# Optimization experiments

Hardware: AMD Instinct MI355X
Metric: run time of the kernel (lower is better)

Reference implementation:

```python
import jax, jax.numpy as jnp
import numpy as np

EPS = 1e-9  # Dice BatchNormalization epsilon


def dice(x, alpha):
    # Keras BatchNormalization(axis=-1, center=False, scale=False) in training
    # mode: normalize over all axes except the last using batch statistics.
    mean = jnp.mean(x, axis=(0, 1), keepdims=True)
    var = jnp.var(x, axis=(0, 1), keepdims=True)
    x_normed = (x - mean) * jax.lax.rsqrt(var + EPS)
    p = jax.nn.sigmoid(x_normed)
    return alpha * (1.0 - p) * x + p * x


def setup_inputs() -> dict:
    key = jax.random.key(0)
    ks = jax.random.split(key, 11)
    B, T, D = 512, 2048, 20
    keys_ = jax.random.normal(ks[0], (B, T, D), dtype=jnp.float32)
    query = jax.random.normal(ks[1], (B, 1, D), dtype=jnp.float32)
    mask = jax.random.randint(ks[2], (B, T), 0, 2) > 0
    # DNN tower weights: hidden dims 80 -> 32 -> 16, attention head 16 -> 1
    W0 = jax.random.normal(ks[3], (80, 32), dtype=jnp.float32) * 0.1
    b0 = jax.random.normal(ks[4], (32,), dtype=jnp.float32) * 0.1
    a0 = jax.random.normal(ks[5], (32,), dtype=jnp.float32) * 0.1
    W1 = jax.random.normal(ks[6], (32, 16), dtype=jnp.float32) * 0.1
    b1 = jax.random.normal(ks[7], (16,), dtype=jnp.float32) * 0.1
    a1 = jax.random.normal(ks[8], (16,), dtype=jnp.float32) * 0.1
    wk = jax.random.normal(ks[9], (16, 1), dtype=jnp.float32) * 0.1
    bk = jax.random.normal(ks[10], (1,), dtype=jnp.float32) * 0.1
    return {"keys": keys_, "query": query, "mask": mask,
            "W0": W0, "b0": b0, "a0": a0,
            "W1": W1, "b1": b1, "a1": a1,
            "wk": wk, "bk": bk}


def reference(keys, query, mask, W0, b0, a0, W1, b1, a1, wk, bk):
    B, T, D = keys.shape
    # repeat query along the key/time axis: [B,1,D] -> [B,T,D]
    queries = jnp.broadcast_to(query, (B, T, D))
    # local-activation features: [B,T,4D] = [B,T,80]
    att = jnp.concatenate([queries, keys, queries - keys, queries * keys], axis=-1)
    # DNN tower with Dice activations (dropout is identity at inference)
    h = dice(att @ W0 + b0, a0)   # [B,T,32]
    h = dice(h @ W1 + b1, a1)     # [B,T,16]
    score = h @ wk + bk           # [B,T,1]
    outputs = jnp.transpose(score, (0, 2, 1))  # [B,1,T]
    # NOTE: the original code computes the masked scores into self.outputs but
    # then (weight_normalization=False, return_score=False) overwrites it with
    # matmul(outputs, keys) using the UNMASKED scores -- we reproduce that.
    return jnp.matmul(outputs, keys)  # [B,1,D]
```

## Files before the change

kernel.cpp:

```cpp
#include <hip/hip_runtime.h>


#define BB 512
#define TT 2048
#define DD 20
#define C0 32
#define C1 16

#define NTH 256
#define NPOS 4
#define POSB (NTH * NPOS)
#define NBLK (TT / POSB)

#define WS_SUM0 0
#define WS_SQ0 32
#define WS_SUM1 64
#define WS_SQ1 80
#define WS_SCALE0 96
#define WS_SHIFT0 128
#define WS_SCALE1 160
#define WS_SHIFT1 176
#define WS_BLOB 192
#define BLOB_J 24
#define BLOB_B (C0 * BLOB_J)

#define PIN(x) asm volatile("" : "+v"(x))

__device__ __forceinline__ float fast_sigmoid(float x) {
    return __builtin_amdgcn_rcpf(1.0f + __expf(-x));
}

__device__ __forceinline__ void load_krow(const float* __restrict__ row,
                                          float* kk) {
    const float4* kr = (const float4*)row;
    float4 a = kr[0], b = kr[1], c = kr[2], d = kr[3], e = kr[4];
    kk[0] = a.x; kk[1] = a.y; kk[2] = a.z; kk[3] = a.w;
    kk[4] = b.x; kk[5] = b.y; kk[6] = b.z; kk[7] = b.w;
    kk[8] = c.x; kk[9] = c.y; kk[10] = c.z; kk[11] = c.w;
    kk[12] = d.x; kk[13] = d.y; kk[14] = d.z; kk[15] = d.w;
    kk[16] = e.x; kk[17] = e.y; kk[18] = e.z; kk[19] = e.w;
}

__global__ void prep_kernel(const float* __restrict__ query,
                            const float* __restrict__ W0,
                            const float* __restrict__ b0,
                            float* __restrict__ blob) {
    const int b = blockIdx.x * 2 + (threadIdx.x >> 5);
    const int j = threadIdx.x & 31;
    float cj = b0[j];
    float* dst = blob + (size_t)b * BLOB_B + j * BLOB_J;
#pragma unroll
    for (int d = 0; d < DD; ++d) {
        float w_q = W0[d * C0 + j];
        float w_k = W0[(DD + d) * C0 + j];
        float w_d = W0[(2 * DD + d) * C0 + j];
        float w_p = W0[(3 * DD + d) * C0 + j];
        float qd = query[b * DD + d];
        dst[d] = w_k - w_d + qd * w_p;
        cj = fmaf(qd, w_q + w_d, cj);
    }
    dst[20] = cj;
}

__global__ __launch_bounds__(256, 2) void pass1_kernel(
    const float* __restrict__ keys, const float* __restrict__ blob,
    float* __restrict__ ws) {
    const int b = blockIdx.x >> 2, chunk = blockIdx.x & 3;
    const int tid = threadIdx.x, wave = tid >> 6, lane = tid & 63;
    const int j0 = wave * 8;
    const float* wb = blob + (size_t)b * BLOB_B;
    const float* kbase = keys + ((size_t)b * TT + chunk * (TT / 4)) * DD;

    float wM[8][DD], cj8[8];
#pragma unroll
    for (int jj = 0; jj < 8; ++jj) {
        load_krow(wb + (j0 + jj) * BLOB_J, wM[jj]);
        cj8[jj] = wb[(j0 + jj) * BLOB_J + 20];
    }
#pragma unroll
    for (int jj = 0; jj < 8; ++jj) {
        PIN(cj8[jj]);
#pragma unroll
        for (int d = 0; d < DD; ++d) PIN(wM[jj][d]);
    }

    float s[8], q[8];
#pragma unroll
    for (int v = 0; v < 8; ++v) { s[v] = 0.f; q[v] = 0.f; }

#pragma unroll 1
    for (int it = 0; it < (TT / 4) / 64; ++it) {
        float kk[DD];
        load_krow(kbase + (size_t)(it * 64 + lane) * DD, kk);
#pragma unroll
        for (int jj = 0; jj < 8; ++jj) {
            float h = cj8[jj];
#pragma unroll
            for (int d = 0; d < DD; ++d) h = fmaf(kk[d], wM[jj][d], h);
            s[jj] += h;
            q[jj] = fmaf(h, h, q[jj]);
        }
    }
    float mine = 0.f;
#pragma unroll
    for (int v = 0; v < 16; ++v) {
        float val = (v < 8) ? s[v] : q[v - 8];
#pragma unroll
        for (int o = 32; o >= 1; o >>= 1) val += __shfl_xor(val, o);
        if (lane == v) mine = val;
    }
    __shared__ float red[64];
    if (lane < 16) {
        int j = j0 + (lane & 7);
        red[(lane < 8 ? 0 : 32) + j] = mine;
    }
    __syncthreads();
    if (tid < 64) atomicAdd(&ws[WS_SUM0 + tid], red[tid]);
}

__global__ void finalize_kernel(float* __restrict__ ws, int nch, int sumOff,
                                int sqOff, int scOff, int shOff) {
    int j = threadIdx.x;
    if (j < nch) {
        const float invN = 1.0f / (float)(BB * TT);
        float mean = ws[sumOff + j] * invN;
        float ex2 = ws[sqOff + j] * invN;
        float var = ex2 - mean * mean;
        float sc = rsqrtf(var + 1e-9f);
        ws[scOff + j] = sc;
        ws[shOff + j] = -mean * sc;
    }
}

#define STAGE_WEIGHTS()                                                      \
    for (int idx = tid; idx < C0 * 24; idx += NTH) {                         \
        int j = idx / 24, r = idx - j * 24;                                  \
        float v;                                                             \
        if (r < 21) v = blob[(size_t)b * BLOB_B + j * BLOB_J + r];           \
        else if (r == 21) v = ws[WS_SCALE0 + j];                             \
        else if (r == 22) v = ws[WS_SHIFT0 + j];                             \
        else v = a0[j];                                                      \
        lw[idx] = v;                                                         \
    }                                                                        \
    for (int idx = tid; idx < C0 * C1; idx += NTH) lw1[idx] = W1[idx];

#define LOAD_AND_PIN_KEYS()                                                  \
    const float* kbase = keys + ((size_t)b * TT + chunk * POSB) * DD;        \
    float kk[NPOS][DD];                                                      \
    _Pragma("unroll") for (int pp = 0; pp < NPOS; ++pp)                      \
        load_krow(kbase + (size_t)(tid + pp * NTH) * DD, kk[pp]);            \
    _Pragma("unroll") for (int pp = 0; pp < NPOS; ++pp)                      \
        _Pragma("unroll") for (int d = 0; d < DD; ++d) PIN(kk[pp][d]);

#define TOWER_JLOOP()                                                        \
    _Pragma("unroll 1") for (int j = 0; j < C0; ++j) {                       \
        const float4* wv = (const float4*)&lw[j * 24];                       \
        float4 A = wv[0], B = wv[1], Cc = wv[2], E = wv[3], F = wv[4],       \
               P = wv[5];                                                    \
        const float4* uv = (const float4*)&lw1[j * C1];                      \
        float4 U0 = uv[0], U1 = uv[1], U2 = uv[2], U3 = uv[3];               \
        float wr[DD] = {A.x,  A.y,  A.z,  A.w,  B.x,  B.y,  B.z,             \
                        B.w,  Cc.x, Cc.y, Cc.z, Cc.w, E.x,  E.y,             \
                        E.z,  E.w,  F.x,  F.y,  F.z,  F.w};                  \
        float ur[C1] = {U0.x, U0.y, U0.z, U0.w, U1.x, U1.y, U1.z, U1.w,      \
                        U2.x, U2.y, U2.z, U2.w, U3.x, U3.y, U3.z, U3.w};     \
        float h[NPOS];                                                       \
        _Pragma("unroll") for (int pp = 0; pp < NPOS; ++pp) {                \
            float hh = P.x;                                                  \
            _Pragma("unroll") for (int d = 0; d < DD; ++d)                   \
                hh = fmaf(kk[pp][d], wr[d], hh);                             \
            h[pp] = hh;                                                      \
        }                                                                    \
        _Pragma("unroll") for (int pp = 0; pp < NPOS; ++pp) {                \
            float pr = fast_sigmoid(fmaf(h[pp], P.y, P.z));                  \
            float h0d = h[pp] * (P.w + pr * (1.0f - P.w));                   \
            _Pragma("unroll") for (int c = 0; c < C1; ++c)                   \
                h1[pp][c] = fmaf(h0d, ur[c], h1[pp][c]);                     \
        }                                                                    \
    }

__global__ __launch_bounds__(NTH, 2) void pass2_kernel(
    const float* __restrict__ keys, const float* __restrict__ blob,
    const float* __restrict__ a0, const float* __restrict__ W1,
    const float* __restrict__ b1, float* __restrict__ ws) {
    const int b = blockIdx.x >> 1, chunk = blockIdx.x & 1;
    const int tid = threadIdx.x, wave = tid >> 6, lane = tid & 63;
    __shared__ float lw[C0 * 24];
    __shared__ float lw1[C0 * C1];
    __shared__ float red[4][32];
    STAGE_WEIGHTS()
    __syncthreads();

    LOAD_AND_PIN_KEYS()

    float h1[NPOS][C1];
#pragma unroll
    for (int pp = 0; pp < NPOS; ++pp)
#pragma unroll
        for (int c = 0; c < C1; ++c) h1[pp][c] = 0.f;

    TOWER_JLOOP()

    float s1[C1], q1[C1];
#pragma unroll
    for (int c = 0; c < C1; ++c) {
        float bc = b1[c], sv = 0.f, qv = 0.f;
#pragma unroll
        for (int pp = 0; pp < NPOS; ++pp) {
            float v = h1[pp][c] + bc;
            sv += v;
            qv = fmaf(v, v, qv);
        }
        s1[c] = sv;
        q1[c] = qv;
    }
    float mine = 0.f;
#pragma unroll
    for (int v = 0; v < 32; ++v) {
        float val = (v < C1) ? s1[v] : q1[v - C1];
#pragma unroll
        for (int o = 32; o >= 1; o >>= 1) val += __shfl_xor(val, o);
        if (lane == v) mine = val;
    }
    if (lane < 32) red[wave][lane] = mine;
    __syncthreads();
    if (tid < 32)
        atomicAdd(&ws[WS_SUM1 + tid],
                  red[0][tid] + red[1][tid] + red[2][tid] + red[3][tid]);
}

__global__ __launch_bounds__(NTH, 2) void pass3_kernel(
    const float* __restrict__ keys, const float* __restrict__ blob,
    const float* __restrict__ a0, const float* __restrict__ W1,
    const float* __restrict__ b1, const float* __restrict__ a1,
    const float* __restrict__ wk, const float* __restrict__ bk,
    const float* __restrict__ ws, float* __restrict__ out) {
    const int b = blockIdx.x >> 1, chunk = blockIdx.x & 1;
    const int tid = threadIdx.x, wave = tid >> 6, lane = tid & 63;
    __shared__ float lw[C0 * 24];
    __shared__ float lw1[C0 * C1];
    __shared__ float ld1[C1 * 4];
    __shared__ float red[4][DD];
    STAGE_WEIGHTS()
    if (tid < C1) {
        ld1[tid * 4 + 0] = ws[WS_SCALE1 + tid];
        ld1[tid * 4 + 1] = ws[WS_SHIFT1 + tid];
        ld1[tid * 4 + 2] = a1[tid];
        ld1[tid * 4 + 3] = wk[tid];
    }
    __syncthreads();

    LOAD_AND_PIN_KEYS()

    float h1[NPOS][C1];
#pragma unroll
    for (int pp = 0; pp < NPOS; ++pp)
#pragma unroll
        for (int c = 0; c < C1; ++c) h1[pp][c] = 0.f;

    TOWER_JLOOP()

    const float bkv = bk[0];
    float oacc[DD];
#pragma unroll
    for (int d = 0; d < DD; ++d) oacc[d] = 0.f;
#pragma unroll
    for (int pp = 0; pp < NPOS; ++pp) {
        float score = bkv;
#pragma unroll
        for (int c = 0; c < C1; ++c) {
            float v = h1[pp][c] + b1[c];
            float pr = fast_sigmoid(fmaf(v, ld1[c * 4 + 0], ld1[c * 4 + 1]));
            float al = ld1[c * 4 + 2];
            float hd = v * (al + pr * (1.0f - al));
            score = fmaf(hd, ld1[c * 4 + 3], score);
        }
#pragma unroll
        for (int d = 0; d < DD; ++d) oacc[d] = fmaf(score, kk[pp][d], oacc[d]);
    }
    float mine = 0.f;
#pragma unroll
    for (int v = 0; v < DD; ++v) {
        float val = oacc[v];
#pragma unroll
        for (int o = 32; o >= 1; o >>= 1) val += __shfl_xor(val, o);
        if (lane == v) mine = val;
    }
    if (lane < DD) red[wave][lane] = mine;
    __syncthreads();
    if (tid < DD)
        atomicAdd(&out[b * DD + tid],
                  red[0][tid] + red[1][tid] + red[2][tid] + red[3][tid]);
}

extern "C" void kernel_launch(void* const* d_in, const int* in_sizes, int n_in,
                              void* d_out, int out_size, void* d_ws,
                              size_t ws_size, hipStream_t stream) {
    const float* keys = (const float*)d_in[0];
    const float* query = (const float*)d_in[1];
    const float* W0 = (const float*)d_in[3];
    const float* b0 = (const float*)d_in[4];
    const float* a0 = (const float*)d_in[5];
    const float* W1 = (const float*)d_in[6];
    const float* b1 = (const float*)d_in[7];
    const float* a1 = (const float*)d_in[8];
    const float* wk = (const float*)d_in[9];
    const float* bk = (const float*)d_in[10];
    float* out = (float*)d_out;
    float* ws = (float*)d_ws;
    float* blob = ws + WS_BLOB;

    hipMemsetAsync(ws, 0, 96 * sizeof(float), stream);
    hipMemsetAsync(out, 0, (size_t)out_size * sizeof(float), stream);

    prep_kernel<<<BB / 2, 64, 0, stream>>>(query, W0, b0, blob);

    pass1_kernel<<<BB * 4, 256, 0, stream>>>(keys, blob, ws);
    finalize_kernel<<<1, 32, 0, stream>>>(ws, 32, WS_SUM0, WS_SQ0, WS_SCALE0,
                                          WS_SHIFT0);
    pass2_kernel<<<BB * NBLK, NTH, 0, stream>>>(keys, blob, a0, W1, b1, ws);
    finalize_kernel<<<1, 16, 0, stream>>>(ws, 16, WS_SUM1, WS_SQ1, WS_SCALE1,
                                          WS_SHIFT1);
    pass3_kernel<<<BB * NBLK, NTH, 0, stream>>>(keys, blob, a0, W1, b1, a1, wk,
                                                bk, ws, out);
}
```

Measured before the change: 288.8 us.

## Fuse prep and finalize kernels into passes, stream weights from LDS with prefetch

Removes the separate prep kernel and the two finalize launches: each pass block now folds the query into W0 itself in shared memory and computes the BatchNorm scale and shift from the raw sums. Pass1 no longer pins 160 weight registers; it reads weights from LDS with a one-row software prefetch and double-buffers the key row loads. The tower j-loop likewise prefetches the next weight row from LDS. This cuts launch count and register pressure, at the cost of redundant per-block weight folding and extra LDS traffic.

```diff
diff --git a/kernel.cpp b/kernel.cpp
--- a/kernel.cpp
+++ b/kernel.cpp
@@ -10,19 +10,12 @@
 #define NTH 256
 #define NPOS 4
 #define POSB (NTH * NPOS)
-#define NBLK (TT / POSB)
 
 #define WS_SUM0 0
 #define WS_SQ0 32
 #define WS_SUM1 64
 #define WS_SQ1 80
-#define WS_SCALE0 96
-#define WS_SHIFT0 128
-#define WS_SCALE1 160
-#define WS_SHIFT1 176
-#define WS_BLOB 192
-#define BLOB_J 24
-#define BLOB_B (C0 * BLOB_J)
+#define EPS 1e-9f
 
 #define PIN(x) asm volatile("" : "+v"(x))
 
@@ -41,48 +34,44 @@
     kk[16] = e.x; kk[17] = e.y; kk[18] = e.z; kk[19] = e.w;
 }
 
-__global__ void prep_kernel(const float* __restrict__ query,
-                            const float* __restrict__ W0,
-                            const float* __restrict__ b0,
-                            float* __restrict__ blob) {
-    const int b = blockIdx.x * 2 + (threadIdx.x >> 5);
-    const int j = threadIdx.x & 31;
-    float cj = b0[j];
-    float* dst = blob + (size_t)b * BLOB_B + j * BLOB_J;
-#pragma unroll
-    for (int d = 0; d < DD; ++d) {
-        float w_q = W0[d * C0 + j];
+__device__ __forceinline__ void stage_fold(int b, int tid,
+                                           const float* __restrict__ query,
+                                           const float* __restrict__ W0,
+                                           const float* __restrict__ b0,
+                                           float* lw) {
+    for (int idx = tid; idx < C0 * DD; idx += NTH) {
+        int j = idx & 31, d = idx >> 5;
+        float qd = query[b * DD + d];
         float w_k = W0[(DD + d) * C0 + j];
         float w_d = W0[(2 * DD + d) * C0 + j];
         float w_p = W0[(3 * DD + d) * C0 + j];
-        float qd = query[b * DD + d];
-        dst[d] = w_k - w_d + qd * w_p;
-        cj = fmaf(qd, w_q + w_d, cj);
-    }
-    dst[20] = cj;
-}
-
-__global__ __launch_bounds__(256, 2) void pass1_kernel(
-    const float* __restrict__ keys, const float* __restrict__ blob,
+        lw[j * 24 + d] = w_k - w_d + qd * w_p;
+    }
+    if (tid < C0) {
+        float cj = b0[tid];
+        for (int d = 0; d < DD; ++d) {
+            float qd = query[b * DD + d];
+            cj = fmaf(qd, W0[d * C0 + tid] + W0[(2 * DD + d) * C0 + tid], cj);
+        }
+        lw[tid * 24 + 20] = cj;
+    }
+}
+
+__global__ __launch_bounds__(NTH, 2) void pass1_kernel(
+    const float* __restrict__ keys, const float* __restrict__ query,
+    const float* __restrict__ W0, const float* __restrict__ b0,
     float* __restrict__ ws) {
     const int b = blockIdx.x >> 2, chunk = blockIdx.x & 3;
     const int tid = threadIdx.x, wave = tid >> 6, lane = tid & 63;
     const int j0 = wave * 8;
-    const float* wb = blob + (size_t)b * BLOB_B;
+    __shared__ float lw[C0 * 24];
+    __shared__ float red[64];
+    stage_fold(b, tid, query, W0, b0, lw);
+    __syncthreads();
+
     const float* kbase = keys + ((size_t)b * TT + chunk * (TT / 4)) * DD;
-
-    float wM[8][DD], cj8[8];
-#pragma unroll
-    for (int jj = 0; jj < 8; ++jj) {
-        load_krow(wb + (j0 + jj) * BLOB_J, wM[jj]);
-        cj8[jj] = wb[(j0 + jj) * BLOB_J + 20];
-    }
-#pragma unroll
-    for (int jj = 0; jj < 8; ++jj) {
-        PIN(cj8[jj]);
-#pragma unroll
-        for (int d = 0; d < DD; ++d) PIN(wM[jj][d]);
-    }
+    float kk[DD], kn[DD];
+    load_krow(kbase + (size_t)lane * DD, kk);
 
     float s[8], q[8];
 #pragma unroll
@@ -90,16 +79,36 @@
 
 #pragma unroll 1
     for (int it = 0; it < (TT / 4) / 64; ++it) {
-        float kk[DD];
-        load_krow(kbase + (size_t)(it * 64 + lane) * DD, kk);
+        if (it < (TT / 4) / 64 - 1)
+            load_krow(kbase + (size_t)((it + 1) * 64 + lane) * DD, kn);
+#pragma unroll
+        for (int d = 0; d < DD; ++d) PIN(kk[d]);
+
+        const float4* wv = (const float4*)&lw[j0 * 24];
+        float4 A = wv[0], B = wv[1], C2 = wv[2], D2 = wv[3], E2 = wv[4],
+               F2 = wv[5];
 #pragma unroll
         for (int jj = 0; jj < 8; ++jj) {
-            float h = cj8[jj];
-#pragma unroll
-            for (int d = 0; d < DD; ++d) h = fmaf(kk[d], wM[jj][d], h);
+            float4 nA, nB, nC, nD, nE, nF;
+            if (jj < 7) {
+                const float4* nv = (const float4*)&lw[(j0 + jj + 1) * 24];
+                nA = nv[0]; nB = nv[1]; nC = nv[2];
+                nD = nv[3]; nE = nv[4]; nF = nv[5];
+            }
+            float wr[DD] = {A.x,  A.y,  A.z,  A.w,  B.x,  B.y,  B.z,
+                            B.w,  C2.x, C2.y, C2.z, C2.w, D2.x, D2.y,
+                            D2.z, D2.w, E2.x, E2.y, E2.z, E2.w};
+            float h = F2.x;
+#pragma unroll
+            for (int d = 0; d < DD; ++d) h = fmaf(kk[d], wr[d], h);
             s[jj] += h;
             q[jj] = fmaf(h, h, q[jj]);
+            if (jj < 7) {
+                A = nA; B = nB; C2 = nC; D2 = nD; E2 = nE; F2 = nF;
+            }
         }
+#pragma unroll
+        for (int d = 0; d < DD; ++d) kk[d] = kn[d];
     }
     float mine = 0.f;
 #pragma unroll
@@ -109,7 +118,6 @@
         for (int o = 32; o >= 1; o >>= 1) val += __shfl_xor(val, o);
         if (lane == v) mine = val;
     }
-    __shared__ float red[64];
     if (lane < 16) {
         int j = j0 + (lane & 7);
         red[(lane < 8 ? 0 : 32) + j] = mine;
@@ -118,31 +126,59 @@
     if (tid < 64) atomicAdd(&ws[WS_SUM0 + tid], red[tid]);
 }
 
-__global__ void finalize_kernel(float* __restrict__ ws, int nch, int sumOff,
-                                int sqOff, int scOff, int shOff) {
-    int j = threadIdx.x;
-    if (j < nch) {
+__device__ __forceinline__ void stage_dice0(int tid,
+                                            const float* __restrict__ ws,
+                                            const float* __restrict__ a0,
+                                            float* lw) {
+    if (tid < C0) {
         const float invN = 1.0f / (float)(BB * TT);
-        float mean = ws[sumOff + j] * invN;
-        float ex2 = ws[sqOff + j] * invN;
-        float var = ex2 - mean * mean;
-        float sc = rsqrtf(var + 1e-9f);
-        ws[scOff + j] = sc;
-        ws[shOff + j] = -mean * sc;
-    }
-}
-
-#define STAGE_WEIGHTS()                                                      \
-    for (int idx = tid; idx < C0 * 24; idx += NTH) {                         \
-        int j = idx / 24, r = idx - j * 24;                                  \
-        float v;                                                             \
-        if (r < 21) v = blob[(size_t)b * BLOB_B + j * BLOB_J + r];           \
-        else if (r == 21) v = ws[WS_SCALE0 + j];                             \
-        else if (r == 22) v = ws[WS_SHIFT0 + j];                             \
-        else v = a0[j];                                                      \
-        lw[idx] = v;                                                         \
+        float mean = ws[WS_SUM0 + tid] * invN;
+        float ex2 = ws[WS_SQ0 + tid] * invN;
+        float sc = rsqrtf(ex2 - mean * mean + EPS);
+        lw[tid * 24 + 21] = sc;
+        lw[tid * 24 + 22] = -mean * sc;
+        lw[tid * 24 + 23] = a0[tid];
+    }
+}
+
+#define TOWER_JLOOP()                                                        \
+    float4 cA, cB, cC, cD, cE, cF;                                           \
+    {                                                                        \
+        const float4* wv = (const float4*)&lw[0];                            \
+        cA = wv[0]; cB = wv[1]; cC = wv[2];                                  \
+        cD = wv[3]; cE = wv[4]; cF = wv[5];                                  \
     }                                                                        \
-    for (int idx = tid; idx < C0 * C1; idx += NTH) lw1[idx] = W1[idx];
+    _Pragma("unroll 1") for (int j = 0; j < C0; ++j) {                       \
+        const float4* uv = (const float4*)&lw1[j * C1];                      \
+        float4 U0 = uv[0], U1 = uv[1], U2 = uv[2], U3 = uv[3];               \
+        float4 nA, nB, nC, nD, nE, nF;                                       \
+        if (j < C0 - 1) {                                                    \
+            const float4* nv = (const float4*)&lw[(j + 1) * 24];             \
+            nA = nv[0]; nB = nv[1]; nC = nv[2];                              \
+            nD = nv[3]; nE = nv[4]; nF = nv[5];                              \
+        }                                                                    \
+        float wr[DD] = {cA.x, cA.y, cA.z, cA.w, cB.x, cB.y, cB.z,            \
+                        cB.w, cC.x, cC.y, cC.z, cC.w, cD.x, cD.y,            \
+                        cD.z, cD.w, cE.x, cE.y, cE.z, cE.w};                 \
+        float h[NPOS];                                                       \
+        _Pragma("unroll") for (int pp = 0; pp < NPOS; ++pp) {                \
+            float hh = cF.x;                                                 \
+            _Pragma("unroll") for (int d = 0; d < DD; ++d)                   \
+                hh = fmaf(kk[pp][d], wr[d], hh);                             \
+            h[pp] = hh;                                                      \
+        }                                                                    \
+        float ur[C1] = {U0.x, U0.y, U0.z, U0.w, U1.x, U1.y, U1.z, U1.w,      \
+                        U2.x, U2.y, U2.z, U2.w, U3.x, U3.y, U3.z, U3.w};     \
+        _Pragma("unroll") for (int pp = 0; pp < NPOS; ++pp) {                \
+            float pr = fast_sigmoid(fmaf(h[pp], cF.y, cF.z));                \
+            float h0d = h[pp] * (cF.w + pr * (1.0f - cF.w));                 \
+            _Pragma("unroll") for (int c = 0; c < C1; ++c)                   \
+                h1[pp][c] = fmaf(h0d, ur[c], h1[pp][c]);                     \
+        }                                                                    \
+        if (j < C0 - 1) {                                                    \
+            cA = nA; cB = nB; cC = nC; cD = nD; cE = nE; cF = nF;            \
+        }                                                                    \
+    }
 
 #define LOAD_AND_PIN_KEYS()                                                  \
     const float* kbase = keys + ((size_t)b * TT + chunk * POSB) * DD;        \
@@ -152,35 +188,9 @@
     _Pragma("unroll") for (int pp = 0; pp < NPOS; ++pp)                      \
         _Pragma("unroll") for (int d = 0; d < DD; ++d) PIN(kk[pp][d]);
 
-#define TOWER_JLOOP()                                                        \
-    _Pragma("unroll 1") for (int j = 0; j < C0; ++j) {                       \
-        const float4* wv = (const float4*)&lw[j * 24];                       \
-        float4 A = wv[0], B = wv[1], Cc = wv[2], E = wv[3], F = wv[4],       \
-               P = wv[5];                                                    \
-        const float4* uv = (const float4*)&lw1[j * C1];                      \
-        float4 U0 = uv[0], U1 = uv[1], U2 = uv[2], U3 = uv[3];               \
-        float wr[DD] = {A.x,  A.y,  A.z,  A.w,  B.x,  B.y,  B.z,             \
-                        B.w,  Cc.x, Cc.y, Cc.z, Cc.w, E.x,  E.y,             \
-                        E.z,  E.w,  F.x,  F.y,  F.z,  F.w};                  \
-        float ur[C1] = {U0.x, U0.y, U0.z, U0.w, U1.x, U1.y, U1.z, U1.w,      \
-                        U2.x, U2.y, U2.z, U2.w, U3.x, U3.y, U3.z, U3.w};     \
-        float h[NPOS];                                                       \
-        _Pragma("unroll") for (int pp = 0; pp < NPOS; ++pp) {                \
-            float hh = P.x;                                                  \
-            _Pragma("unroll") for (int d = 0; d < DD; ++d)                   \
-                hh = fmaf(kk[pp][d], wr[d], hh);                             \
-            h[pp] = hh;                                                      \
-        }                                                                    \
-        _Pragma("unroll") for (int pp = 0; pp < NPOS; ++pp) {                \
-            float pr = fast_sigmoid(fmaf(h[pp], P.y, P.z));                  \
-            float h0d = h[pp] * (P.w + pr * (1.0f - P.w));                   \
-            _Pragma("unroll") for (int c = 0; c < C1; ++c)                   \
-                h1[pp][c] = fmaf(h0d, ur[c], h1[pp][c]);                     \
-        }                                                                    \
-    }
-
 __global__ __launch_bounds__(NTH, 2) void pass2_kernel(
-    const float* __restrict__ keys, const float* __restrict__ blob,
+    const float* __restrict__ keys, const float* __restrict__ query,
+    const float* __restrict__ W0, const float* __restrict__ b0,
     const float* __restrict__ a0, const float* __restrict__ W1,
     const float* __restrict__ b1, float* __restrict__ ws) {
     const int b = blockIdx.x >> 1, chunk = blockIdx.x & 1;
@@ -188,7 +198,9 @@
     __shared__ float lw[C0 * 24];
     __shared__ float lw1[C0 * C1];
     __shared__ float red[4][32];
-    STAGE_WEIGHTS()
+    stage_fold(b, tid, query, W0, b0, lw);
+    stage_dice0(tid, ws, a0, lw);
+    for (int idx = tid; idx < C0 * C1; idx += NTH) lw1[idx] = W1[idx];
     __syncthreads();
 
     LOAD_AND_PIN_KEYS()
@@ -230,7 +242,8 @@
 }
 
 __global__ __launch_bounds__(NTH, 2) void pass3_kernel(
-    const float* __restrict__ keys, const float* __restrict__ blob,
+    const float* __restrict__ keys, const float* __restrict__ query,
+    const float* __restrict__ W0, const float* __restrict__ b0,
     const float* __restrict__ a0, const float* __restrict__ W1,
     const float* __restrict__ b1, const float* __restrict__ a1,
     const float* __restrict__ wk, const float* __restrict__ bk,
@@ -241,10 +254,16 @@
     __shared__ float lw1[C0 * C1];
     __shared__ float ld1[C1 * 4];
     __shared__ float red[4][DD];
-    STAGE_WEIGHTS()
+    stage_fold(b, tid, query, W0, b0, lw);
+    stage_dice0(tid, ws, a0, lw);
+    for (int idx = tid; idx < C0 * C1; idx += NTH) lw1[idx] = W1[idx];
     if (tid < C1) {
-        ld1[tid * 4 + 0] = ws[WS_SCALE1 + tid];
-        ld1[tid * 4 + 1] = ws[WS_SHIFT1 + tid];
+        const float invN = 1.0f / (float)(BB * TT);
+        float mean = ws[WS_SUM1 + tid] * invN;
+        float ex2 = ws[WS_SQ1 + tid] * invN;
+        float sc = rsqrtf(ex2 - mean * mean + EPS);
+        ld1[tid * 4 + 0] = sc;
+        ld1[tid * 4 + 1] = -mean * sc;
         ld1[tid * 4 + 2] = a1[tid];
         ld1[tid * 4 + 3] = wk[tid];
     }
@@ -308,19 +327,13 @@
     const float* bk = (const float*)d_in[10];
     float* out = (float*)d_out;
     float* ws = (float*)d_ws;
-    float* blob = ws + WS_BLOB;
 
     hipMemsetAsync(ws, 0, 96 * sizeof(float), stream);
     hipMemsetAsync(out, 0, (size_t)out_size * sizeof(float), stream);
 
-    prep_kernel<<<BB / 2, 64, 0, stream>>>(query, W0, b0, blob);
-
-    pass1_kernel<<<BB * 4, 256, 0, stream>>>(keys, blob, ws);
-    finalize_kernel<<<1, 32, 0, stream>>>(ws, 32, WS_SUM0, WS_SQ0, WS_SCALE0,
-                                          WS_SHIFT0);
-    pass2_kernel<<<BB * NBLK, NTH, 0, stream>>>(keys, blob, a0, W1, b1, ws);
-    finalize_kernel<<<1, 16, 0, stream>>>(ws, 16, WS_SUM1, WS_SQ1, WS_SCALE1,
-                                          WS_SHIFT1);
-    pass3_kernel<<<BB * NBLK, NTH, 0, stream>>>(keys, blob, a0, W1, b1, a1, wk,
-                                                bk, ws, out);
-}
+    pass1_kernel<<<BB * 4, NTH, 0, stream>>>(keys, query, W0, b0, ws);
+    pass2_kernel<<<BB * 2, NTH, 0, stream>>>(keys, query, W0, b0, a0, W1, b1,
+                                             ws);
+    pass3_kernel<<<BB * 2, NTH, 0, stream>>>(keys, query, W0, b0, a0, W1, b1,
+                                             a1, wk, bk, ws, out);
+}
```

New measurement: 313.2 us. +8.5%, slower.

## Fold BN finalize into consumers, read weights directly, restructure pass1 per-thread

Applied to the files above, without the earlier changes.

Drops the two single-block finalize kernels; each consumer block now computes the Dice batch-norm scale and shift from the raw sums itself. The pass2/pass3 tower loop reads layer weights straight from global memory (uniform loads) instead of staging them in LDS. pass1 switches from a wave-per-8-channels layout with a loop over positions to each thread holding two key rows and computing all 32 channels with 64 wave reductions. This removes launch gaps and LDS staging, but adds redundant normalization math per block, more scalar or global weight traffic, and a heavier shuffle reduction in pass1.

```diff
diff --git a/kernel.cpp b/kernel.cpp
--- a/kernel.cpp
+++ b/kernel.cpp
@@ -10,19 +10,15 @@
 #define NTH 256
 #define NPOS 4
 #define POSB (NTH * NPOS)
-#define NBLK (TT / POSB)
 
 #define WS_SUM0 0
 #define WS_SQ0 32
 #define WS_SUM1 64
 #define WS_SQ1 80
-#define WS_SCALE0 96
-#define WS_SHIFT0 128
-#define WS_SCALE1 160
-#define WS_SHIFT1 176
 #define WS_BLOB 192
 #define BLOB_J 24
 #define BLOB_B (C0 * BLOB_J)
+#define EPS 1e-9f
 
 #define PIN(x) asm volatile("" : "+v"(x))
 
@@ -62,87 +58,54 @@
     dst[20] = cj;
 }
 
-__global__ __launch_bounds__(256, 2) void pass1_kernel(
+__global__ __launch_bounds__(NTH, 2) void pass1_kernel(
     const float* __restrict__ keys, const float* __restrict__ blob,
     float* __restrict__ ws) {
     const int b = blockIdx.x >> 2, chunk = blockIdx.x & 3;
     const int tid = threadIdx.x, wave = tid >> 6, lane = tid & 63;
-    const int j0 = wave * 8;
+    const float* kbase = keys + ((size_t)b * TT + chunk * (TT / 4)) * DD;
     const float* wb = blob + (size_t)b * BLOB_B;
-    const float* kbase = keys + ((size_t)b * TT + chunk * (TT / 4)) * DD;
-
-    float wM[8][DD], cj8[8];
-#pragma unroll
-    for (int jj = 0; jj < 8; ++jj) {
-        load_krow(wb + (j0 + jj) * BLOB_J, wM[jj]);
-        cj8[jj] = wb[(j0 + jj) * BLOB_J + 20];
-    }
-#pragma unroll
-    for (int jj = 0; jj < 8; ++jj) {
-        PIN(cj8[jj]);
-#pragma unroll
-        for (int d = 0; d < DD; ++d) PIN(wM[jj][d]);
-    }
-
-    float s[8], q[8];
-#pragma unroll
-    for (int v = 0; v < 8; ++v) { s[v] = 0.f; q[v] = 0.f; }
-
-#pragma unroll 1
-    for (int it = 0; it < (TT / 4) / 64; ++it) {
-        float kk[DD];
-        load_krow(kbase + (size_t)(it * 64 + lane) * DD, kk);
-#pragma unroll
-        for (int jj = 0; jj < 8; ++jj) {
-            float h = cj8[jj];
-#pragma unroll
-            for (int d = 0; d < DD; ++d) h = fmaf(kk[d], wM[jj][d], h);
-            s[jj] += h;
-            q[jj] = fmaf(h, h, q[jj]);
+
+    float kk[2][DD];
+    load_krow(kbase + (size_t)tid * DD, kk[0]);
+    load_krow(kbase + (size_t)(tid + NTH) * DD, kk[1]);
+#pragma unroll
+    for (int pp = 0; pp < 2; ++pp)
+#pragma unroll
+        for (int d = 0; d < DD; ++d) PIN(kk[pp][d]);
+
+    float s[C0], q[C0];
+#pragma unroll
+    for (int j = 0; j < C0; ++j) { s[j] = 0.f; q[j] = 0.f; }
+
+#pragma unroll
+    for (int j = 0; j < C0; ++j) {
+        const float* w = wb + j * BLOB_J;
+        float h0 = w[20], h1v = w[20];
+#pragma unroll
+        for (int d = 0; d < DD; ++d) {
+            h0 = fmaf(kk[0][d], w[d], h0);
+            h1v = fmaf(kk[1][d], w[d], h1v);
         }
+        s[j] += h0 + h1v;
+        q[j] = fmaf(h0, h0, q[j]);
+        q[j] = fmaf(h1v, h1v, q[j]);
     }
     float mine = 0.f;
 #pragma unroll
-    for (int v = 0; v < 16; ++v) {
-        float val = (v < 8) ? s[v] : q[v - 8];
+    for (int v = 0; v < 64; ++v) {
+        float val = (v < C0) ? s[v] : q[v - C0];
 #pragma unroll
         for (int o = 32; o >= 1; o >>= 1) val += __shfl_xor(val, o);
         if (lane == v) mine = val;
     }
-    __shared__ float red[64];
-    if (lane < 16) {
-        int j = j0 + (lane & 7);
-        red[(lane < 8 ? 0 : 32) + j] = mine;
-    }
-    __syncthreads();
-    if (tid < 64) atomicAdd(&ws[WS_SUM0 + tid], red[tid]);
-}
-
-__global__ void finalize_kernel(float* __restrict__ ws, int nch, int sumOff,
-                                int sqOff, int scOff, int shOff) {
-    int j = threadIdx.x;
-    if (j < nch) {
-        const float invN = 1.0f / (float)(BB * TT);
-        float mean = ws[sumOff + j] * invN;
-        float ex2 = ws[sqOff + j] * invN;
-        float var = ex2 - mean * mean;
-        float sc = rsqrtf(var + 1e-9f);
-        ws[scOff + j] = sc;
-        ws[shOff + j] = -mean * sc;
-    }
-}
-
-#define STAGE_WEIGHTS()                                                      \
-    for (int idx = tid; idx < C0 * 24; idx += NTH) {                         \
-        int j = idx / 24, r = idx - j * 24;                                  \
-        float v;                                                             \
-        if (r < 21) v = blob[(size_t)b * BLOB_B + j * BLOB_J + r];           \
-        else if (r == 21) v = ws[WS_SCALE0 + j];                             \
-        else if (r == 22) v = ws[WS_SHIFT0 + j];                             \
-        else v = a0[j];                                                      \
-        lw[idx] = v;                                                         \
-    }                                                                        \
-    for (int idx = tid; idx < C0 * C1; idx += NTH) lw1[idx] = W1[idx];
+    __shared__ float red[4][64];
+    red[wave][lane] = mine;
+    __syncthreads();
+    if (tid < 64)
+        atomicAdd(&ws[tid],
+                  red[0][tid] + red[1][tid] + red[2][tid] + red[3][tid]);
+}
 
 #define LOAD_AND_PIN_KEYS()                                                  \
     const float* kbase = keys + ((size_t)b * TT + chunk * POSB) * DD;        \
@@ -153,30 +116,33 @@
         _Pragma("unroll") for (int d = 0; d < DD; ++d) PIN(kk[pp][d]);
 
 #define TOWER_JLOOP()                                                        \
-    _Pragma("unroll 1") for (int j = 0; j < C0; ++j) {                       \
-        const float4* wv = (const float4*)&lw[j * 24];                       \
-        float4 A = wv[0], B = wv[1], Cc = wv[2], E = wv[3], F = wv[4],       \
-               P = wv[5];                                                    \
-        const float4* uv = (const float4*)&lw1[j * C1];                      \
-        float4 U0 = uv[0], U1 = uv[1], U2 = uv[2], U3 = uv[3];               \
-        float wr[DD] = {A.x,  A.y,  A.z,  A.w,  B.x,  B.y,  B.z,             \
-                        B.w,  Cc.x, Cc.y, Cc.z, Cc.w, E.x,  E.y,             \
-                        E.z,  E.w,  F.x,  F.y,  F.z,  F.w};                  \
-        float ur[C1] = {U0.x, U0.y, U0.z, U0.w, U1.x, U1.y, U1.z, U1.w,      \
-                        U2.x, U2.y, U2.z, U2.w, U3.x, U3.y, U3.z, U3.w};     \
+    _Pragma("unroll 2") for (int j = 0; j < C0; ++j) {                       \
+        float4 P = ld0[j];            \
+        const float* w = wb + j * BLOB_J;             \
+        const float* u = W1 + j * C1;                 \
         float h[NPOS];                                                       \
         _Pragma("unroll") for (int pp = 0; pp < NPOS; ++pp) {                \
             float hh = P.x;                                                  \
             _Pragma("unroll") for (int d = 0; d < DD; ++d)                   \
-                hh = fmaf(kk[pp][d], wr[d], hh);                             \
+                hh = fmaf(kk[pp][d], w[d], hh);                              \
             h[pp] = hh;                                                      \
         }                                                                    \
         _Pragma("unroll") for (int pp = 0; pp < NPOS; ++pp) {                \
             float pr = fast_sigmoid(fmaf(h[pp], P.y, P.z));                  \
             float h0d = h[pp] * (P.w + pr * (1.0f - P.w));                   \
             _Pragma("unroll") for (int c = 0; c < C1; ++c)                   \
-                h1[pp][c] = fmaf(h0d, ur[c], h1[pp][c]);                     \
+                h1[pp][c] = fmaf(h0d, u[c], h1[pp][c]);                      \
         }                                                                    \
+    }
+
+#define STAGE_DICE0()                                                        \
+    if (tid < C0) {                                                          \
+        const float invN = 1.0f / (float)(BB * TT);                          \
+        float mean = ws[WS_SUM0 + tid] * invN;                               \
+        float ex2 = ws[WS_SQ0 + tid] * invN;                                 \
+        float sc = rsqrtf(ex2 - mean * mean + EPS);                          \
+        ld0[tid] = make_float4(blob[(size_t)b * BLOB_B + tid * BLOB_J + 20], \
+                               sc, -mean * sc, a0[tid]);                     \
     }
 
 __global__ __launch_bounds__(NTH, 2) void pass2_kernel(
@@ -185,10 +151,10 @@
     const float* __restrict__ b1, float* __restrict__ ws) {
     const int b = blockIdx.x >> 1, chunk = blockIdx.x & 1;
     const int tid = threadIdx.x, wave = tid >> 6, lane = tid & 63;
-    __shared__ float lw[C0 * 24];
-    __shared__ float lw1[C0 * C1];
+    const float* wb = blob + (size_t)b * BLOB_B;
+    __shared__ float4 ld0[C0];
     __shared__ float red[4][32];
-    STAGE_WEIGHTS()
+    STAGE_DICE0()
     __syncthreads();
 
     LOAD_AND_PIN_KEYS()
@@ -237,16 +203,17 @@
     const float* __restrict__ ws, float* __restrict__ out) {
     const int b = blockIdx.x >> 1, chunk = blockIdx.x & 1;
     const int tid = threadIdx.x, wave = tid >> 6, lane = tid & 63;
-    __shared__ float lw[C0 * 24];
-    __shared__ float lw1[C0 * C1];
-    __shared__ float ld1[C1 * 4];
+    const float* wb = blob + (size_t)b * BLOB_B;
+    __shared__ float4 ld0[C0];
+    __shared__ float4 ld1[C1];
     __shared__ float red[4][DD];
-    STAGE_WEIGHTS()
+    STAGE_DICE0()
     if (tid < C1) {
-        ld1[tid * 4 + 0] = ws[WS_SCALE1 + tid];
-        ld1[tid * 4 + 1] = ws[WS_SHIFT1 + tid];
-        ld1[tid * 4 + 2] = a1[tid];
-        ld1[tid * 4 + 3] = wk[tid];
+        const float invN = 1.0f / (float)(BB * TT);
+        float mean = ws[WS_SUM1 + tid] * invN;
+        float ex2 = ws[WS_SQ1 + tid] * invN;
+        float sc = rsqrtf(ex2 - mean * mean + EPS);
+        ld1[tid] = make_float4(sc, -mean * sc, a1[tid], wk[tid]);
     }
     __syncthreads();
 
@@ -270,10 +237,10 @@
 #pragma unroll
         for (int c = 0; c < C1; ++c) {
             float v = h1[pp][c] + b1[c];
-            float pr = fast_sigmoid(fmaf(v, ld1[c * 4 + 0], ld1[c * 4 + 1]));
-            float al = ld1[c * 4 + 2];
-            float hd = v * (al + pr * (1.0f - al));
-            score = fmaf(hd, ld1[c * 4 + 3], score);
+            float4 Q = ld1[c];
+            float pr = fast_sigmoid(fmaf(v, Q.x, Q.y));
+            float hd = v * (Q.z + pr * (1.0f - Q.z));
+            score = fmaf(hd, Q.w, score);
         }
 #pragma unroll
         for (int d = 0; d < DD; ++d) oacc[d] = fmaf(score, kk[pp][d], oacc[d]);
@@ -315,12 +282,8 @@
 
     prep_kernel<<<BB / 2, 64, 0, stream>>>(query, W0, b0, blob);
 
-    pass1_kernel<<<BB * 4, 256, 0, stream>>>(keys, blob, ws);
-    finalize_kernel<<<1, 32, 0, stream>>>(ws, 32, WS_SUM0, WS_SQ0, WS_SCALE0,
-                                          WS_SHIFT0);
-    pass2_kernel<<<BB * NBLK, NTH, 0, stream>>>(keys, blob, a0, W1, b1, ws);
-    finalize_kernel<<<1, 16, 0, stream>>>(ws, 16, WS_SUM1, WS_SQ1, WS_SCALE1,
-                                          WS_SHIFT1);
-    pass3_kernel<<<BB * NBLK, NTH, 0, stream>>>(keys, blob, a0, W1, b1, a1, wk,
-                                                bk, ws, out);
-}
+    pass1_kernel<<<BB * 4, NTH, 0, stream>>>(keys, blob, ws);
+    pass2_kernel<<<BB * 2, NTH, 0, stream>>>(keys, blob, a0, W1, b1, ws);
+    pass3_kernel<<<BB * 2, NTH, 0, stream>>>(keys, blob, a0, W1, b1, a1, wk,
+                                             bk, ws, out);
+}
```

New measurement: 298.5 us. +3.4%, slower.
